# Performance work log

Hardware: AMD Instinct MI355X
Metric: run time of the kernel (lower is better)

## Reference

```python
import jax, jax.numpy as jnp
import numpy as np
import itertools

F = 20        # field_size
D = 16        # embedding_size / output_dims
H = 2         # num_hash
NB = 500000   # num_buckets
B = 4096      # batch
NI = F * (F - 1) // 2  # 190 pairwise interactions


def _interact_indexes(field_size):
    # For each field i, indices of the C(F,2) combinations that contain i -> [F, F-1]
    combos = list(itertools.combinations(range(field_size), 2))
    idx = [[j for j, c in enumerate(combos) if i in c] for i in range(field_size)]
    return np.asarray(idx, dtype=np.int32)


def setup_inputs() -> dict:
    key = jax.random.key(0)
    k0, k1, k2, k3, k4, k5 = jax.random.split(key, 6)
    return {
        "origin_embeddings": jax.random.normal(k0, (B, F, D), jnp.float32),
        "codebook": jax.random.normal(k1, (NB, D), jnp.float32) * 0.01,
        "W_transform": jax.random.normal(k2, (H * D, D), jnp.float32) * 0.05,
        "senet_w1": jax.random.normal(k3, (F * D, F * D), jnp.float32) * 0.02,
        "senet_w2": jax.random.normal(k4, (F * D, NI), jnp.float32) * 0.02,
        # Precomputed hash bucket ids (stands in for the StrongHash of string tokens)
        "hash_idx": jax.random.randint(k5, (H, B, NI), 0, NB, dtype=jnp.int32),
        "interact_indexes": jnp.asarray(_interact_indexes(F)),
    }


def reference(origin_embeddings, codebook, W_transform, senet_w1, senet_w2, hash_idx, interact_indexes):
    b = origin_embeddings.shape[0]
    # multi-hash codebook gathers (hash-share: one codebook): [H, B, NI, D]
    gathered = codebook[hash_idx]
    # merge_mode='concat' over hash functions -> [B, NI, H*D]
    emb = jnp.concatenate([gathered[i] for i in range(gathered.shape[0])], axis=-1)
    # hash_merge_final_transform: Dense(output_dims, no bias) -> [B, NI, D]
    emb = jnp.einsum('bne,ed->bnd', emb, W_transform)
    # SENET (bit squeeze, ratio 1.0, vector excitation, no activation) over origin embeddings
    z = origin_embeddings.reshape(b, -1)          # [B, F*D]
    w = (z @ senet_w1) @ senet_w2                 # [B, NI]
    # gather each field's interactions and weighted-sum ('senetsum')
    field_emb = emb[:, interact_indexes]          # [B, F, F-1, D]
    field_w = w[:, interact_indexes][..., None]   # [B, F, F-1, 1]
    out = jnp.sum(field_emb * field_w, axis=-2)   # [B, F, D]
    return out
```

## Files before the change

### kernel.cpp

```cpp
#include <hip/hip_runtime.h>

#define FF 20
#define NI 190
#define NIP 192
#define BB 4096
#define FD 320
#define PV 20

__global__ __launch_bounds__(192) void k_w12(const float* __restrict__ w1,
                                             const float* __restrict__ w2,
                                             float* __restrict__ W12p) {
    __shared__ float srow[FD];
    int r = blockIdx.x;
    for (int j = threadIdx.x; j < FD; j += 192) srow[j] = w1[r * FD + j];
    __syncthreads();
    int c = threadIdx.x;
    float acc = 0.f;
    if (c < NI) {
        for (int k = 0; k < FD; ++k) acc += srow[k] * w2[k * NI + c];
    }
    W12p[r * NIP + c] = acc;
}

__global__ __launch_bounds__(256) void k_w(const float* __restrict__ z,
                                           const float* __restrict__ W12p,
                                           float* __restrict__ wout) {
    __shared__ float zT[32][68];
    __shared__ float Ws[32][64];
    int b0 = blockIdx.x * 64;
    int c0 = blockIdx.y * 64;
    int t = threadIdx.x;
    int tr = t >> 4, tc = t & 15;
    float acc[4][4];
#pragma unroll
    for (int i = 0; i < 4; ++i)
#pragma unroll
        for (int j = 0; j < 4; ++j) acc[i][j] = 0.f;

    for (int k0 = 0; k0 < FD; k0 += 32) {
#pragma unroll
        for (int s = 0; s < 2; ++s) {
            int task = t + s * 256;
            int row = task >> 3, ch = task & 7;
            float4 v = *(const float4*)&z[(b0 + row) * FD + k0 + ch * 4];
            zT[ch * 4 + 0][row] = v.x;
            zT[ch * 4 + 1][row] = v.y;
            zT[ch * 4 + 2][row] = v.z;
            zT[ch * 4 + 3][row] = v.w;
        }
#pragma unroll
        for (int s = 0; s < 2; ++s) {
            int task = t + s * 256;
            int kr = task >> 4, cq = task & 15;
            *(float4*)&Ws[kr][cq * 4] = *(const float4*)&W12p[(k0 + kr) * NIP + c0 + cq * 4];
        }
        __syncthreads();
#pragma unroll
        for (int k = 0; k < 32; ++k) {
            float4 zb = *(const float4*)&zT[k][tr * 4];
            float4 wv = *(const float4*)&Ws[k][tc * 4];
            float zz[4] = {zb.x, zb.y, zb.z, zb.w};
            float ww[4] = {wv.x, wv.y, wv.z, wv.w};
#pragma unroll
            for (int i = 0; i < 4; ++i)
#pragma unroll
                for (int j = 0; j < 4; ++j) acc[i][j] += zz[i] * ww[j];
        }
        __syncthreads();
    }
#pragma unroll
    for (int i = 0; i < 4; ++i) {
        float4 v = make_float4(acc[i][0], acc[i][1], acc[i][2], acc[i][3]);
        *(float4*)&wout[(b0 + tr * 4 + i) * NIP + c0 + tc * 4] = v;
    }
}

#define SA(f, h, d) ((f) * 33 + (h) * 16 + (d))
__global__ __launch_bounds__(320) void k_main(const float* __restrict__ cb,
                                              const float* __restrict__ Wt,
                                              const int* __restrict__ hidx,
                                              const int* __restrict__ iidx,
                                              const float* __restrict__ wbuf,
                                              float* __restrict__ out) {
    __shared__ int s_i0[NI], s_i1[NI];
    __shared__ float s_w[NI];
    __shared__ int s_plist[FF * 19];
    __shared__ float s_W[32 * 16];
    __shared__ __align__(16) float s_v[NI * PV];
    __shared__ float s_acc[19 * 33 + 2 * 16 + 16];

    int t = threadIdx.x;
    int b = blockIdx.x;

    if (t < NI) {
        s_i0[t] = hidx[b * NI + t];
        s_i1[t] = hidx[(BB + b) * NI + t];
        s_w[t] = wbuf[b * NIP + t];
    }
    for (int j = t; j < FF * 19; j += 320) s_plist[j] = iidx[j];
    for (int j = t; j < 512; j += 320) s_W[j] = Wt[j];
    __syncthreads();

    const float4* cb4 = (const float4*)cb;
    int q  = t & 3;
    int pb = t >> 2;
    bool has3 = pb < (NI - 160);

    float4 g0a = cb4[s_i0[pb] * 4 + q];
    float4 g0b = cb4[s_i0[pb + 80] * 4 + q];
    float4 g0c;
    if (has3) g0c = cb4[s_i0[pb + 160] * 4 + q];
    float w_a = s_w[pb], w_b = s_w[pb + 80];
    float w_c = has3 ? s_w[pb + 160] : 0.f;

    *(float4*)&s_v[pb * PV + q * 4] =
        make_float4(g0a.x * w_a, g0a.y * w_a, g0a.z * w_a, g0a.w * w_a);
    *(float4*)&s_v[(pb + 80) * PV + q * 4] =
        make_float4(g0b.x * w_b, g0b.y * w_b, g0b.z * w_b, g0b.w * w_b);
    if (has3)
        *(float4*)&s_v[(pb + 160) * PV + q * 4] =
            make_float4(g0c.x * w_c, g0c.y * w_c, g0c.z * w_c, g0c.w * w_c);
    __syncthreads();

    float4 g1a = cb4[s_i1[pb] * 4 + q];
    float4 g1b = cb4[s_i1[pb + 80] * 4 + q];
    float4 g1c;
    if (has3) g1c = cb4[s_i1[pb + 160] * 4 + q];

    int f = t >> 4, d = t & 15;
    const int* pl = &s_plist[f * 19];
    float a0 = 0.f;
#pragma unroll
    for (int j = 0; j < 19; ++j) a0 += s_v[pl[j] * PV + d];
    __syncthreads();

    *(float4*)&s_v[pb * PV + q * 4] =
        make_float4(g1a.x * w_a, g1a.y * w_a, g1a.z * w_a, g1a.w * w_a);
    *(float4*)&s_v[(pb + 80) * PV + q * 4] =
        make_float4(g1b.x * w_b, g1b.y * w_b, g1b.z * w_b, g1b.w * w_b);
    if (has3)
        *(float4*)&s_v[(pb + 160) * PV + q * 4] =
            make_float4(g1c.x * w_c, g1c.y * w_c, g1c.z * w_c, g1c.w * w_c);
    __syncthreads();

    float a1 = 0.f;
#pragma unroll
    for (int j = 0; j < 19; ++j) a1 += s_v[pl[j] * PV + d];

    s_acc[SA(f, 0, d)] = a0;
    s_acc[SA(f, 1, d)] = a1;
    __syncthreads();

    float r = 0.f;
#pragma unroll
    for (int k = 0; k < 16; ++k) {
        r += s_acc[SA(f, 0, k)] * s_W[k * 16 + d];
        r += s_acc[SA(f, 1, k)] * s_W[(16 + k) * 16 + d];
    }
    out[b * FD + t] = r;
}

extern "C" void kernel_launch(void* const* d_in, const int* in_sizes, int n_in,
                              void* d_out, int out_size, void* d_ws, size_t ws_size,
                              hipStream_t stream) {
    const float* origin = (const float*)d_in[0];
    const float* cb     = (const float*)d_in[1];
    const float* Wt     = (const float*)d_in[2];
    const float* w1     = (const float*)d_in[3];
    const float* w2     = (const float*)d_in[4];
    const int*   hidx   = (const int*)d_in[5];
    const int*   iidx   = (const int*)d_in[6];
    float* out = (float*)d_out;

    float* W12p = (float*)d_ws;
    float* wbuf = W12p + FD * NIP;

    k_w12<<<FD, 192, 0, stream>>>(w1, w2, W12p);
    dim3 gw(BB / 64, 3);
    k_w<<<gw, 256, 0, stream>>>(origin, W12p, wbuf);
    k_main<<<BB, 320, 0, stream>>>(cb, Wt, hidx, iidx, wbuf, out);
}
```

Measured before the change: 143.3 us.

## Restructure SENET weight GEMM with wave-uniform W loads and double-buffered z tiles

The z@W12 GEMM kernel is rewritten so that each wavefront handles 8 output columns for 64 batch rows. The W12 values are now read as wave-uniform loads straight from global memory (scalar/broadcast) instead of staged through shared memory. z tiles are double-buffered in LDS with prefetch of the next k-slice, leaving one barrier per step. The grid grows from 3 to 6 column blocks, which raises parallelism, but each thread now does more register FMAs per loaded z value and less reuse of the output tile.

```diff
diff --git a/kernel.cpp b/kernel.cpp
--- a/kernel.cpp
+++ b/kernel.cpp
@@ -25,54 +25,60 @@
 __global__ __launch_bounds__(256) void k_w(const float* __restrict__ z,
                                            const float* __restrict__ W12p,
                                            float* __restrict__ wout) {
-    __shared__ float zT[32][68];
-    __shared__ float Ws[32][64];
+    __shared__ float4 zb[2][8][64];
+    int t = threadIdx.x;
     int b0 = blockIdx.x * 64;
-    int c0 = blockIdx.y * 64;
-    int t = threadIdx.x;
-    int tr = t >> 4, tc = t & 15;
-    float acc[4][4];
-#pragma unroll
-    for (int i = 0; i < 4; ++i)
-#pragma unroll
-        for (int j = 0; j < 4; ++j) acc[i][j] = 0.f;
+    int c0 = blockIdx.y * 32;
+    int wv = __builtin_amdgcn_readfirstlane(t >> 6);
+    int lane = t & 63;
+    int cw = c0 + wv * 8;
+    const float* __restrict__ Wk = W12p + cw;
 
-    for (int k0 = 0; k0 < FD; k0 += 32) {
-#pragma unroll
-        for (int s = 0; s < 2; ++s) {
-            int task = t + s * 256;
-            int row = task >> 3, ch = task & 7;
-            float4 v = *(const float4*)&z[(b0 + row) * FD + k0 + ch * 4];
-            zT[ch * 4 + 0][row] = v.x;
-            zT[ch * 4 + 1][row] = v.y;
-            zT[ch * 4 + 2][row] = v.z;
-            zT[ch * 4 + 3][row] = v.w;
+    int ka = t & 7,        ra = t >> 3;
+    int kb = t & 7,        rb = (t >> 3) + 32;
+
+    float acc[8] = {0.f, 0.f, 0.f, 0.f, 0.f, 0.f, 0.f, 0.f};
+
+    {
+        float4 va = *(const float4*)&z[(size_t)(b0 + ra) * FD + ka * 4];
+        float4 vb = *(const float4*)&z[(size_t)(b0 + rb) * FD + kb * 4];
+        zb[0][ka][ra] = va;
+        zb[0][kb][rb] = vb;
+    }
+    __syncthreads();
+
+    int buf = 0;
+    for (int step = 0; step < 10; ++step) {
+        int k0 = step * 32;
+        float4 va, vb;
+        if (step < 9) {
+            va = *(const float4*)&z[(size_t)(b0 + ra) * FD + (k0 + 32) + ka * 4];
+            vb = *(const float4*)&z[(size_t)(b0 + rb) * FD + (k0 + 32) + kb * 4];
         }
 #pragma unroll
-        for (int s = 0; s < 2; ++s) {
-            int task = t + s * 256;
-            int kr = task >> 4, cq = task & 15;
-            *(float4*)&Ws[kr][cq * 4] = *(const float4*)&W12p[(k0 + kr) * NIP + c0 + cq * 4];
+        for (int kg = 0; kg < 8; ++kg) {
+            float4 zf = zb[buf][kg][lane];
+            float zz[4] = {zf.x, zf.y, zf.z, zf.w};
+#pragma unroll
+            for (int kk = 0; kk < 4; ++kk) {
+                const float* __restrict__ wr = Wk + (size_t)(k0 + kg * 4 + kk) * NIP;
+                float zkv = zz[kk];
+#pragma unroll
+                for (int j = 0; j < 8; ++j) acc[j] = fmaf(zkv, wr[j], acc[j]);
+            }
         }
-        __syncthreads();
-#pragma unroll
-        for (int k = 0; k < 32; ++k) {
-            float4 zb = *(const float4*)&zT[k][tr * 4];
-            float4 wv = *(const float4*)&Ws[k][tc * 4];
-            float zz[4] = {zb.x, zb.y, zb.z, zb.w};
-            float ww[4] = {wv.x, wv.y, wv.z, wv.w};
-#pragma unroll
-            for (int i = 0; i < 4; ++i)
-#pragma unroll
-                for (int j = 0; j < 4; ++j) acc[i][j] += zz[i] * ww[j];
+        if (step < 9) {
+            zb[buf ^ 1][ka][ra] = va;
+            zb[buf ^ 1][kb][rb] = vb;
+            __syncthreads();
+            buf ^= 1;
         }
-        __syncthreads();
     }
-#pragma unroll
-    for (int i = 0; i < 4; ++i) {
-        float4 v = make_float4(acc[i][0], acc[i][1], acc[i][2], acc[i][3]);
-        *(float4*)&wout[(b0 + tr * 4 + i) * NIP + c0 + tc * 4] = v;
-    }
+
+    float4 o0 = make_float4(acc[0], acc[1], acc[2], acc[3]);
+    float4 o1 = make_float4(acc[4], acc[5], acc[6], acc[7]);
+    *(float4*)&wout[(size_t)(b0 + lane) * NIP + cw] = o0;
+    *(float4*)&wout[(size_t)(b0 + lane) * NIP + cw + 4] = o1;
 }
 
 #define SA(f, h, d) ((f) * 33 + (h) * 16 + (d))
@@ -176,7 +182,7 @@
     float* wbuf = W12p + FD * NIP;
 
     k_w12<<<FD, 192, 0, stream>>>(w1, w2, W12p);
-    dim3 gw(BB / 64, 3);
+    dim3 gw(BB / 64, NIP / 32);
     k_w<<<gw, 256, 0, stream>>>(origin, W12p, wbuf);
     k_main<<<BB, 320, 0, stream>>>(cb, Wt, hidx, iidx, wbuf, out);
 }
```

After: 150.0 us. 1.05x slower.

## Split-K the SENET weight GEMMs and software-prefetch the k_w tiles

Applied to the files above, without the earlier changes.

k_w12 is split into two K halves over a 2D grid, each writing its own partial W12 product. k_w now sums the two halves as it loads its tiles, adds a split-K of 4 via grid z, and uses register double-buffered prefetching with a smaller 16-wide K tile. k_main sums the four partial w buffers when it loads its weights. The aim is more blocks and better latency hiding in the small precompute kernels, at the cost of extra workspace traffic and redundant partial-sum reads.

```diff
diff --git a/kernel.cpp b/kernel.cpp
--- a/kernel.cpp
+++ b/kernel.cpp
@@ -6,29 +6,35 @@
 #define BB 4096
 #define FD 320
 #define PV 20
+#define KH 160
+#define KQ 80
 
 __global__ __launch_bounds__(192) void k_w12(const float* __restrict__ w1,
                                              const float* __restrict__ w2,
                                              float* __restrict__ W12p) {
-    __shared__ float srow[FD];
+    __shared__ float srow[KH];
     int r = blockIdx.x;
-    for (int j = threadIdx.x; j < FD; j += 192) srow[j] = w1[r * FD + j];
+    int h = blockIdx.y;
+    int k0 = h * KH;
+    for (int j = threadIdx.x; j < KH; j += 192) srow[j] = w1[r * FD + k0 + j];
     __syncthreads();
     int c = threadIdx.x;
     float acc = 0.f;
     if (c < NI) {
-        for (int k = 0; k < FD; ++k) acc += srow[k] * w2[k * NI + c];
-    }
-    W12p[r * NIP + c] = acc;
+        for (int k = 0; k < KH; ++k) acc += srow[k] * w2[(k0 + k) * NI + c];
+    }
+    W12p[h * (FD * NIP) + r * NIP + c] = acc;
 }
 
 __global__ __launch_bounds__(256) void k_w(const float* __restrict__ z,
                                            const float* __restrict__ W12p,
                                            float* __restrict__ wout) {
-    __shared__ float zT[32][68];
-    __shared__ float Ws[32][64];
+    __shared__ float zT[16][68];
+    __shared__ float Ws[16][64];
+    const float* __restrict__ W12b = W12p + FD * NIP;
     int b0 = blockIdx.x * 64;
     int c0 = blockIdx.y * 64;
+    int kbase = blockIdx.z * KQ;
     int t = threadIdx.x;
     int tr = t >> 4, tc = t & 15;
     float acc[4][4];
@@ -37,26 +43,29 @@
 #pragma unroll
         for (int j = 0; j < 4; ++j) acc[i][j] = 0.f;
 
-    for (int k0 = 0; k0 < FD; k0 += 32) {
-#pragma unroll
-        for (int s = 0; s < 2; ++s) {
-            int task = t + s * 256;
-            int row = task >> 3, ch = task & 7;
-            float4 v = *(const float4*)&z[(b0 + row) * FD + k0 + ch * 4];
-            zT[ch * 4 + 0][row] = v.x;
-            zT[ch * 4 + 1][row] = v.y;
-            zT[ch * 4 + 2][row] = v.z;
-            zT[ch * 4 + 3][row] = v.w;
+    int zrow = t >> 2, zch = t & 3;
+    int kr = t >> 4,  cq = t & 15;
+
+    float4 vz = *(const float4*)&z[(b0 + zrow) * FD + kbase + zch * 4];
+    float4 va = *(const float4*)&W12p[(kbase + kr) * NIP + c0 + cq * 4];
+    float4 vb = *(const float4*)&W12b[(kbase + kr) * NIP + c0 + cq * 4];
+    zT[zch * 4 + 0][zrow] = vz.x;
+    zT[zch * 4 + 1][zrow] = vz.y;
+    zT[zch * 4 + 2][zrow] = vz.z;
+    zT[zch * 4 + 3][zrow] = vz.w;
+    *(float4*)&Ws[kr][cq * 4] =
+        make_float4(va.x + vb.x, va.y + vb.y, va.z + vb.z, va.w + vb.w);
+    __syncthreads();
+
+    for (int ks = 0; ks < KQ; ks += 16) {
+        bool more = (ks + 16) < KQ;
+        if (more) {
+            vz = *(const float4*)&z[(b0 + zrow) * FD + kbase + (ks + 16) + zch * 4];
+            va = *(const float4*)&W12p[(kbase + ks + 16 + kr) * NIP + c0 + cq * 4];
+            vb = *(const float4*)&W12b[(kbase + ks + 16 + kr) * NIP + c0 + cq * 4];
         }
 #pragma unroll
-        for (int s = 0; s < 2; ++s) {
-            int task = t + s * 256;
-            int kr = task >> 4, cq = task & 15;
-            *(float4*)&Ws[kr][cq * 4] = *(const float4*)&W12p[(k0 + kr) * NIP + c0 + cq * 4];
-        }
-        __syncthreads();
-#pragma unroll
-        for (int k = 0; k < 32; ++k) {
+        for (int k = 0; k < 16; ++k) {
             float4 zb = *(const float4*)&zT[k][tr * 4];
             float4 wv = *(const float4*)&Ws[k][tc * 4];
             float zz[4] = {zb.x, zb.y, zb.z, zb.w};
@@ -66,12 +75,22 @@
 #pragma unroll
                 for (int j = 0; j < 4; ++j) acc[i][j] += zz[i] * ww[j];
         }
-        __syncthreads();
+        if (more) {
+            __syncthreads();
+            zT[zch * 4 + 0][zrow] = vz.x;
+            zT[zch * 4 + 1][zrow] = vz.y;
+            zT[zch * 4 + 2][zrow] = vz.z;
+            zT[zch * 4 + 3][zrow] = vz.w;
+            *(float4*)&Ws[kr][cq * 4] =
+                make_float4(va.x + vb.x, va.y + vb.y, va.z + vb.z, va.w + vb.w);
+            __syncthreads();
+        }
     }
 #pragma unroll
     for (int i = 0; i < 4; ++i) {
         float4 v = make_float4(acc[i][0], acc[i][1], acc[i][2], acc[i][3]);
-        *(float4*)&wout[(b0 + tr * 4 + i) * NIP + c0 + tc * 4] = v;
+        *(float4*)&wout[(size_t)blockIdx.z * (BB * NIP) +
+                        (b0 + tr * 4 + i) * NIP + c0 + tc * 4] = v;
     }
 }
 
@@ -95,7 +114,9 @@
     if (t < NI) {
         s_i0[t] = hidx[b * NI + t];
         s_i1[t] = hidx[(BB + b) * NI + t];
-        s_w[t] = wbuf[b * NIP + t];
+        s_w[t] = wbuf[b * NIP + t] + wbuf[(size_t)BB * NIP + b * NIP + t]
+               + wbuf[2 * (size_t)BB * NIP + b * NIP + t]
+               + wbuf[3 * (size_t)BB * NIP + b * NIP + t];
     }
     for (int j = t; j < FF * 19; j += 320) s_plist[j] = iidx[j];
     for (int j = t; j < 512; j += 320) s_W[j] = Wt[j];
@@ -173,10 +194,10 @@
     float* out = (float*)d_out;
 
     float* W12p = (float*)d_ws;
-    float* wbuf = W12p + FD * NIP;
-
-    k_w12<<<FD, 192, 0, stream>>>(w1, w2, W12p);
-    dim3 gw(BB / 64, 3);
+    float* wbuf = W12p + 2 * FD * NIP;
+
+    k_w12<<<dim3(FD, 2), 192, 0, stream>>>(w1, w2, W12p);
+    dim3 gw(BB / 64, 3, 4);
     k_w<<<gw, 256, 0, stream>>>(origin, W12p, wbuf);
     k_main<<<BB, 320, 0, stream>>>(cb, Wt, hidx, iidx, wbuf, out);
 }
```

After: 134.7 us. 6.0% less time.
